# Kernel optimization log

Measured on AMD Instinct MI355X. Metric: run time of the kernel, lower is better.

The kernel has to match this reference:

```python
import jax, jax.numpy as jnp
import numpy as np

NUM_BINS = 10
BIN_DISP = 0.5
MIN_REG = 1e-5
H = 22
W = 22
S = 16
C = 256
F_ = H * W


def _distance_map(center, sz):
    # DiMP DistanceMap: soft-binned radial distance from center. [bins, sz0, sz1]
    bins = jnp.arange(NUM_BINS, dtype=jnp.float32)[:, None, None]
    k0 = jnp.arange(sz[0], dtype=jnp.float32)[:, None]
    k1 = jnp.arange(sz[1], dtype=jnp.float32)[None, :]
    dist = jnp.sqrt((k0 - center[0]) ** 2 + (k1 - center[1]) ** 2)
    bd = dist[None] / BIN_DISP - bins
    lower = jax.nn.relu(1.0 - jnp.abs(bd[:-1]))
    last = jnp.clip(1.0 + bd[-1:], 0.0, 1.0)
    return jnp.concatenate([lower, last], axis=0)


def _unfold_map(fm, h, w):
    # Equivalent of F.unfold(full_map,(h,w)).view(h,w,h,w).flip((2,3)).permute(2,3,0,1):
    # out[f=(li,lj), ki, kj] = fm[h-1-li+ki, w-1-lj+kj]
    r = (h - 1 - jnp.arange(h))[:, None] + jnp.arange(h)[None, :]  # [li, ki]
    c = (w - 1 - jnp.arange(w))[:, None] + jnp.arange(w)[None, :]  # [lj, kj]
    m = fm[r[:, None, :, None], c[None, :, None, :]]  # [li, lj, ki, kj]
    return m.reshape(h * w, h, w)


def setup_inputs() -> dict:
    key = jax.random.key(0)
    k1, k2 = jax.random.split(key)
    filt = jax.random.normal(k1, (S, F_, C, 1, 1), jnp.float32) * 0.1
    feat = jax.random.normal(k2, (1, S, C, H, W), jnp.float32)
    d = jnp.arange(NUM_BINS, dtype=jnp.float32) * BIN_DISP
    init_gauss = jnp.exp(-0.5 * d ** 2)  # init_gauss_sigma = 1.0
    return {
        "filt": filt,
        "feat": feat,
        "log_step_length": jnp.zeros((1,), jnp.float32),          # log(1.0)
        "filter_reg": 0.01 * jnp.ones((1,), jnp.float32),
        "label_w": init_gauss - init_gauss.min(),                  # label_map_predictor weights
        "mask_w": 4.0 * jnp.tanh(2.0 - d),                         # target_mask_predictor weights
        "spatial_w": jnp.ones((NUM_BINS,), jnp.float32),           # spatial_weight_predictor weights
        "num_iter": 3,
    }


def _forward(filt, feat, log_step_length, filter_reg, label_w, mask_w, spatial_w, num_iter):
    f2 = feat[0]            # [S, C, H, W]
    w = filt[..., 0, 0]     # [S, F, C]   (1x1 DiCor filters)
    h, wd = feat.shape[-2], feat.shape[-1]
    s, fnum = w.shape[0], w.shape[1]
    sz = (2 * h - 1, 2 * wd - 1)
    center = jnp.array([sz[0] // 2, sz[1] // 2], dtype=jnp.float32)
    dmap = _distance_map(center, sz)  # [bins, 2H-1, 2W-1]
    # 1x1 convs over the bin dimension, then unfold into per-filter maps [F, H, W]
    label_map = _unfold_map(jnp.einsum('bhw,b->hw', dmap, label_w), h, wd)
    target_mask = _unfold_map(jax.nn.sigmoid(jnp.einsum('bhw,b->hw', dmap, mask_w)), h, wd)
    spatial_weight = _unfold_map(jnp.einsum('bhw,b->hw', dmap, spatial_w), h, wd)
    step_length = jnp.exp(log_step_length[0])
    reg_weight = jnp.maximum(filter_reg[0] * filter_reg[0], MIN_REG ** 2)
    a = target_mask
    sw2 = spatial_weight * spatial_weight
    for _ in range(num_iter):
        # apply_filter with 1x1 filters: scores[s,f,h,w] = sum_c feat[s,c,h,w] * w[s,f,c]
        scores = jnp.einsum('schw,sfc->sfhw', f2, w)
        # LeakyReluPar / LeakyReluParDeriv with per-location slope a
        scores_act = 0.5 * (1.0 - a) * jnp.abs(scores) + 0.5 * (1.0 + a) * scores
        score_mask = 0.5 * (1.0 - a) * jnp.sign(scores) + 0.5 * (1.0 + a)
        residuals = score_mask * (sw2 * (scores_act - label_map))
        # apply_feat_transpose with 1x1 filters
        w_grad = jnp.einsum('sfhw,schw->sfc', residuals, f2) + reg_weight * w
        scores_grad = jnp.einsum('schw,sfc->sfhw', f2, w_grad)
        scores_grad = spatial_weight * (score_mask * scores_grad)
        alpha_num = jnp.sum(w_grad * w_grad, axis=2)  # [S, F]
        alpha_den = jnp.maximum(
            jnp.sum((scores_grad * scores_grad).reshape(s, fnum, -1), axis=2)
            + reg_weight * alpha_num, 1e-8)
        alpha = alpha_num / alpha_den
        w = w - step_length * alpha[..., None] * w_grad
    return w[..., None, None]  # [S, F, C, 1, 1]


def reference(filt, feat, log_step_length, filter_reg, label_w, mask_w, spatial_w, num_iter):
    return _forward(filt, feat, log_step_length, filter_reg, label_w, mask_w, spatial_w, num_iter)
```

## Files before the change

kernel.cpp:

```cpp
#include <hip/hip_runtime.h>
#include <math.h>
#include <stdint.h>

#define Ww 22
#define P_ 484
#define S_ 16
#define C_ 256
#define MP2 234256
#define TSZ 1849

typedef _Float16 f16x8 __attribute__((ext_vector_type(8)));
typedef _Float16 f16x4 __attribute__((ext_vector_type(4)));
typedef float f32x4 __attribute__((ext_vector_type(4)));

__device__ __forceinline__ int xcd_chunk(int bid, int chunk) {
    return (bid & 7) * chunk + (bid >> 3);
}

__device__ __forceinline__ void gld16(const _Float16* g, _Float16* lds) {
    auto* lp = (__attribute__((address_space(3))) uint32_t*)(uintptr_t)(lds);
    auto* gp = (const __attribute__((address_space(1))) uint32_t*)(uintptr_t)(g);
    __builtin_amdgcn_global_load_lds(gp, lp, 16, 0, 0);
}

__global__ void k_maps(const float* __restrict__ label_w, const float* __restrict__ mask_w,
                       const float* __restrict__ spatial_w, f32x4* __restrict__ map4t) {
    int idx = blockIdx.x * blockDim.x + threadIdx.x;
    if (idx >= TSZ) return;
    int dx = idx / 43 - 21, dy = idx % 43 - 21;
    float d = sqrtf((float)(dx * dx + dy * dy)) * 2.0f;
    float lab = 0.f, msk = 0.f, spw = 0.f;
#pragma unroll
    for (int b = 0; b < 9; ++b) {
        float wb = fmaxf(0.f, 1.f - fabsf(d - (float)b));
        lab += wb * label_w[b];
        msk += wb * mask_w[b];
        spw += wb * spatial_w[b];
    }
    float w9 = fminf(fmaxf(1.f + (d - 9.f), 0.f), 1.f);
    lab += w9 * label_w[9];
    msk += w9 * mask_w[9];
    spw += w9 * spatial_w[9];
    f32x4 o;
    o[0] = lab;
    o[1] = 1.f / (1.f + expf(-msk));
    o[2] = spw * spw;
    o[3] = spw;
    map4t[idx] = o;
}

__global__ __launch_bounds__(256) void k_winit(const float* __restrict__ filt,
                                               float* __restrict__ Wf, _Float16* __restrict__ Wh,
                                               float* __restrict__ num, float* __restrict__ den) {
    int wgid = xcd_chunk(blockIdx.x, 256);
    int s = wgid >> 7;
    int t = threadIdx.x;
    int f = (wgid & 127) * 4 + (t >> 6);
    int c = (t & 63) * 4;
    size_t oh = ((size_t)(s * 512 + f)) * C_ + c;
    if (f < P_) {
        size_t o = ((size_t)(s * P_ + f)) * C_ + c;
        f32x4 v = *(const f32x4*)(filt + o);
        *(f32x4*)(Wf + o) = v;
        f16x4 h;
#pragma unroll
        for (int q = 0; q < 4; ++q) h[q] = (_Float16)v[q];
        *(f16x4*)(Wh + oh) = h;
        if ((t & 63) == 0) { num[s * P_ + f] = 0.f; den[s * P_ + f] = 0.f; }
    } else {
        f16x4 h = {};
        *(f16x4*)(Wh + oh) = h;
    }
}

__global__ __launch_bounds__(256) void k_trans(const float* __restrict__ feat,
                                               _Float16* __restrict__ f2h,
                                               _Float16* __restrict__ f2th) {
    int wgid = xcd_chunk(blockIdx.x, 256);
    int s = wgid >> 7;
    int rem = wgid & 127;
    int p0 = (rem & 15) * 32, c0 = (rem >> 4) * 32;
    int cc = threadIdx.x & 31, rr = threadIdx.x >> 5;
    __shared__ float tb[32][33];
#pragma unroll
    for (int q = 0; q < 4; ++q) {
        int c = c0 + rr + q * 8;
        int p = p0 + cc;
        float v = (p < P_) ? feat[((size_t)s * C_ + c) * P_ + p] : 0.f;
        f2h[((size_t)s * C_ + c) * 512 + p] = (_Float16)v;
        tb[rr + q * 8][cc] = v;
    }
    __syncthreads();
#pragma unroll
    for (int q = 0; q < 4; ++q) {
        int p = p0 + rr + q * 8;
        f2th[((size_t)s * 512 + p) * C_ + c0 + cc] = (_Float16)tb[cc][rr + q * 8];
    }
}

template <int EPI, int KK, int LDA, int LDB, int TPS, int NBN>
__global__ __launch_bounds__(256, 4) void k_gemm(
    const _Float16* __restrict__ Ah, const _Float16* __restrict__ Bh,
    const f32x4* __restrict__ map4t, const _Float16* __restrict__ maskh_i,
    const _Float16* __restrict__ Wh_i, const float* __restrict__ freg,
    _Float16* __restrict__ out_h, _Float16* __restrict__ out_h2,
    float* __restrict__ red) {
    constexpr int TI = 2, TJ = 2, NT = KK / 128;
    int tid = threadIdx.x;
    int w = tid >> 6, l = tid & 63;
    int wgid = xcd_chunk(blockIdx.x, S_ * TPS / 8);
    int s = wgid / TPS;
    int rem = wgid % TPS;
    int m0 = (rem / NBN) * 64, n0 = (rem % NBN) * 64;
    int wm = w >> 1, wn = w & 1;
    int r16 = l & 15;

    __shared__ _Float16 As[64 * 128];
    __shared__ _Float16 Bs[64 * 128];

    int lrow = w * 4 + (l >> 4);
    int gsrc = ((l & 15) ^ lrow) << 3;
    const _Float16* gA = Ah + (size_t)s * (512 * LDA) + (size_t)(m0 + lrow) * LDA + gsrc;
    const _Float16* gB = Bh + (size_t)s * 131072 + (size_t)(n0 + lrow) * LDB + gsrc;

    f32x4 acc[TI][TJ] = {};

#pragma unroll
    for (int t = 0; t < NT; ++t) {
#pragma unroll
        for (int i = 0; i < 4; ++i) {
            gld16(gA + (size_t)i * 16 * LDA + t * 128, &As[(i * 16 + w * 4) * 128]);
            gld16(gB + (size_t)i * 16 * LDB + t * 128, &Bs[(i * 16 + w * 4) * 128]);
        }
        __syncthreads();
#pragma unroll
        for (int kk = 0; kk < 4; ++kk) {
            int px = ((kk * 4 + (l >> 4)) ^ r16) << 3;
            f16x8 af[TI], bf[TJ];
#pragma unroll
            for (int ti = 0; ti < TI; ++ti)
                af[ti] = *(const f16x8*)&As[(wm * 32 + ti * 16 + r16) * 128 + px];
#pragma unroll
            for (int tj = 0; tj < TJ; ++tj)
                bf[tj] = *(const f16x8*)&Bs[(wn * 32 + tj * 16 + r16) * 128 + px];
#pragma unroll
            for (int ti = 0; ti < TI; ++ti)
#pragma unroll
                for (int tj = 0; tj < TJ; ++tj)
                    acc[ti][tj] = __builtin_amdgcn_mfma_f32_16x16x32_f16(
                        af[ti], bf[tj], acc[ti][tj], 0, 0, 0);
        }
        if (t + 1 < NT) __syncthreads();
    }

    int q4 = (l >> 4) * 4;

    if constexpr (EPI == 1) {
#pragma unroll
        for (int ti = 0; ti < TI; ++ti)
#pragma unroll
            for (int r = 0; r < 4; ++r) {
                int m = m0 + wm * 32 + ti * 16 + q4 + r;
                int im = m / 22, jm = m - im * 22;
#pragma unroll
                for (int tj = 0; tj < TJ; ++tj) {
                    int n = n0 + wn * 32 + tj * 16 + r16;
                    float res = 0.f;
                    if (m < P_ && n < P_) {
                        int kn = n / 22, ln = n - kn * 22;
                        f32x4 m4 = map4t[(kn - im + 21) * 43 + (ln - jm + 21)];
                        float sc = acc[ti][tj][r];
                        float sgn = (sc > 0.f) ? 1.f : ((sc < 0.f) ? -1.f : 0.f);
                        float msk = 0.5f * (1.f - m4[1]) * sgn + 0.5f * (1.f + m4[1]);
                        res = msk * (m4[2] * (msk * sc - m4[0]));
                        out_h2[(size_t)s * MP2 + (size_t)m * P_ + n] = (_Float16)msk;
                    }
                    out_h[((size_t)(s * 512 + m)) * 512 + n] = (_Float16)res;
                }
            }
    } else if constexpr (EPI == 2) {
        float fr = freg[0];
        float regw = fmaxf(fr * fr, 1e-10f);
#pragma unroll
        for (int ti = 0; ti < TI; ++ti)
#pragma unroll
            for (int r = 0; r < 4; ++r) {
                int m = m0 + wm * 32 + ti * 16 + q4 + r;
                float v = 0.f;
#pragma unroll
                for (int tj = 0; tj < TJ; ++tj) {
                    int n = n0 + wn * 32 + tj * 16 + r16;
                    size_t o = ((size_t)(s * 512 + m)) * C_ + n;
                    float wg = acc[ti][tj][r] + regw * (float)Wh_i[o];
                    out_h[o] = (_Float16)wg;
                    v += wg * wg;
                }
                v += __shfl_xor(v, 1);
                v += __shfl_xor(v, 2);
                v += __shfl_xor(v, 4);
                v += __shfl_xor(v, 8);
                if (r16 == 0 && m < P_) atomicAdd(&red[s * P_ + m], v);
            }
    } else {
#pragma unroll
        for (int ti = 0; ti < TI; ++ti)
#pragma unroll
            for (int r = 0; r < 4; ++r) {
                int m = m0 + wm * 32 + ti * 16 + q4 + r;
                int im = m / 22, jm = m - im * 22;
                float v = 0.f;
#pragma unroll
                for (int tj = 0; tj < TJ; ++tj) {
                    int n = n0 + wn * 32 + tj * 16 + r16;
                    if (m < P_ && n < P_) {
                        int kn = n / 22, ln = n - kn * 22;
                        float spw = map4t[(kn - im + 21) * 43 + (ln - jm + 21)][3];
                        float msk = (float)maskh_i[(size_t)s * MP2 + (size_t)m * P_ + n];
                        float sg = spw * msk * acc[ti][tj][r];
                        v += sg * sg;
                    }
                }
                v += __shfl_xor(v, 1);
                v += __shfl_xor(v, 2);
                v += __shfl_xor(v, 4);
                v += __shfl_xor(v, 8);
                if (r16 == 0 && m < P_) atomicAdd(&red[s * P_ + m], v);
            }
    }
}

__global__ __launch_bounds__(256) void k_update(float* __restrict__ Wf,
                                                const _Float16* __restrict__ wgradh,
                                                float* __restrict__ num, float* __restrict__ den,
                                                const float* __restrict__ freg,
                                                const float* __restrict__ lsl,
                                                _Float16* __restrict__ Wh) {
    int wgid = xcd_chunk(blockIdx.x, 242);
    int s = wgid / 121;
    int t = threadIdx.x;
    int f = (wgid % 121) * 4 + (t >> 6);
    int row = s * P_ + f;
    float nu = num[row], de = den[row];
    float fr = freg[0];
    float regw = fmaxf(fr * fr, 1e-10f);
    float alpha = nu / fmaxf(de + regw * nu, 1e-8f);
    float sa = expf(lsl[0]) * alpha;
    int c = (t & 63) * 4;
    size_t o = (size_t)row * C_ + c;
    size_t oh = ((size_t)(s * 512 + f)) * C_ + c;
    f32x4 wv = *(const f32x4*)(Wf + o);
    f16x4 g = *(const f16x4*)(wgradh + oh);
    f16x4 h;
#pragma unroll
    for (int q = 0; q < 4; ++q) {
        wv[q] -= sa * (float)g[q];
        h[q] = (_Float16)wv[q];
    }
    *(f32x4*)(Wf + o) = wv;
    *(f16x4*)(Wh + oh) = h;
    if ((t & 63) == 0) { num[row] = 0.f; den[row] = 0.f; }
}

extern "C" void kernel_launch(void* const* d_in, const int* in_sizes, int n_in,
                              void* d_out, int out_size, void* d_ws, size_t ws_size,
                              hipStream_t stream) {
    const float* filt = (const float*)d_in[0];
    const float* feat = (const float*)d_in[1];
    const float* lsl  = (const float*)d_in[2];
    const float* freg = (const float*)d_in[3];
    const float* lw   = (const float*)d_in[4];
    const float* mw   = (const float*)d_in[5];
    const float* sw   = (const float*)d_in[6];
    float* Wf = (float*)d_out;

    char* ws = (char*)d_ws;
    f32x4* map4t     = (f32x4*)ws;      ws += (size_t)TSZ * 16;
    _Float16* residh = (_Float16*)ws;   ws += (size_t)S_ * 512 * 512 * 2;
    _Float16* wgradh = (_Float16*)ws;   ws += (size_t)S_ * 512 * C_ * 2;
    _Float16* Wh     = (_Float16*)ws;   ws += (size_t)S_ * 512 * C_ * 2;
    _Float16* f2h    = (_Float16*)ws;   ws += (size_t)S_ * C_ * 512 * 2;
    _Float16* f2th   = (_Float16*)ws;   ws += (size_t)S_ * 512 * C_ * 2;
    _Float16* maskh  = (_Float16*)ws;   ws += (size_t)S_ * MP2 * 2;
    float* num       = (float*)ws;      ws += (size_t)S_ * P_ * 4;
    float* den       = (float*)ws;      ws += (size_t)S_ * P_ * 4;

    k_maps<<<8, 256, 0, stream>>>(lw, mw, sw, map4t);
    k_winit<<<2048, 256, 0, stream>>>(filt, Wf, Wh, num, den);
    k_trans<<<2048, 256, 0, stream>>>(feat, f2h, f2th);

    for (int it = 0; it < 3; ++it) {
        k_gemm<1, 256, 256, 256, 64, 8><<<1024, 256, 0, stream>>>(
            Wh, f2th, map4t, nullptr, nullptr, nullptr, residh, maskh, nullptr);
        k_gemm<2, 512, 512, 512, 32, 4><<<512, 256, 0, stream>>>(
            residh, f2h, map4t, nullptr, Wh, freg, wgradh, nullptr, num);
        k_gemm<3, 256, 256, 256, 64, 8><<<1024, 256, 0, stream>>>(
            wgradh, f2th, map4t, maskh, nullptr, nullptr, nullptr, nullptr, den);
        k_update<<<1936, 256, 0, stream>>>(Wf, wgradh, num, den, freg, lsl, Wh);
    }
}
```

Measured before the change: 140.1 us.

## Update scores linearly from raw score gradient instead of recomputing score GEMM

Because scores are linear in the filter, the new scores after a step equal the old scores minus step*alpha times the raw scores_grad GEMM output, which is already computed. The code stores raw scores and raw score gradients in fp16 and updates scores elementwise in a fused update kernel, which also recomputes the mask and residual. This removes two of the three score GEMMs. The three prologue kernels are merged into one launch, and num/den use ping-pong buffers. In exchange it writes and reads several extra 512x512 fp16 planes per sequence, and fp16 rounding error can accumulate in the score updates.

```diff
diff --git a/kernel.cpp b/kernel.cpp
--- a/kernel.cpp
+++ b/kernel.cpp
@@ -6,7 +6,6 @@
 #define P_ 484
 #define S_ 16
 #define C_ 256
-#define MP2 234256
 #define TSZ 1849
 
 typedef _Float16 f16x8 __attribute__((ext_vector_type(8)));
@@ -23,12 +22,8 @@
     __builtin_amdgcn_global_load_lds(gp, lp, 16, 0, 0);
 }
 
-__global__ void k_maps(const float* __restrict__ label_w, const float* __restrict__ mask_w,
-                       const float* __restrict__ spatial_w, f32x4* __restrict__ map4t) {
-    int idx = blockIdx.x * blockDim.x + threadIdx.x;
-    if (idx >= TSZ) return;
-    int dx = idx / 43 - 21, dy = idx % 43 - 21;
-    float d = sqrtf((float)(dx * dx + dy * dy)) * 2.0f;
+__device__ __forceinline__ f32x4 map_entry(const float* label_w, const float* mask_w,
+                                           const float* spatial_w, float d) {
     float lab = 0.f, msk = 0.f, spw = 0.f;
 #pragma unroll
     for (int b = 0; b < 9; ++b) {
@@ -46,65 +41,78 @@
     o[1] = 1.f / (1.f + expf(-msk));
     o[2] = spw * spw;
     o[3] = spw;
-    map4t[idx] = o;
-}
-
-__global__ __launch_bounds__(256) void k_winit(const float* __restrict__ filt,
-                                               float* __restrict__ Wf, _Float16* __restrict__ Wh,
-                                               float* __restrict__ num, float* __restrict__ den) {
-    int wgid = xcd_chunk(blockIdx.x, 256);
-    int s = wgid >> 7;
+    return o;
+}
+
+__global__ __launch_bounds__(256) void k_pro(
+    const float* __restrict__ filt, const float* __restrict__ feat,
+    const float* __restrict__ lw, const float* __restrict__ mw,
+    const float* __restrict__ sw,
+    float* __restrict__ Wf, _Float16* __restrict__ Wh,
+    float* __restrict__ num0, float* __restrict__ den0,
+    _Float16* __restrict__ f2h, _Float16* __restrict__ f2th,
+    f32x4* __restrict__ map4t) {
+    int wgid = xcd_chunk(blockIdx.x, 514);
+    int x = wgid / 514;
+    int local = wgid % 514;
     int t = threadIdx.x;
-    int f = (wgid & 127) * 4 + (t >> 6);
-    int c = (t & 63) * 4;
-    size_t oh = ((size_t)(s * 512 + f)) * C_ + c;
-    if (f < P_) {
-        size_t o = ((size_t)(s * P_ + f)) * C_ + c;
-        f32x4 v = *(const f32x4*)(filt + o);
-        *(f32x4*)(Wf + o) = v;
-        f16x4 h;
-#pragma unroll
-        for (int q = 0; q < 4; ++q) h[q] = (_Float16)v[q];
-        *(f16x4*)(Wh + oh) = h;
-        if ((t & 63) == 0) { num[s * P_ + f] = 0.f; den[s * P_ + f] = 0.f; }
-    } else {
-        f16x4 h = {};
-        *(f16x4*)(Wh + oh) = h;
-    }
-}
-
-__global__ __launch_bounds__(256) void k_trans(const float* __restrict__ feat,
-                                               _Float16* __restrict__ f2h,
-                                               _Float16* __restrict__ f2th) {
-    int wgid = xcd_chunk(blockIdx.x, 256);
-    int s = wgid >> 7;
-    int rem = wgid & 127;
-    int p0 = (rem & 15) * 32, c0 = (rem >> 4) * 32;
-    int cc = threadIdx.x & 31, rr = threadIdx.x >> 5;
-    __shared__ float tb[32][33];
-#pragma unroll
-    for (int q = 0; q < 4; ++q) {
-        int c = c0 + rr + q * 8;
-        int p = p0 + cc;
-        float v = (p < P_) ? feat[((size_t)s * C_ + c) * P_ + p] : 0.f;
-        f2h[((size_t)s * C_ + c) * 512 + p] = (_Float16)v;
-        tb[rr + q * 8][cc] = v;
-    }
-    __syncthreads();
-#pragma unroll
-    for (int q = 0; q < 4; ++q) {
-        int p = p0 + rr + q * 8;
-        f2th[((size_t)s * 512 + p) * C_ + c0 + cc] = (_Float16)tb[cc][rr + q * 8];
-    }
-}
-
-template <int EPI, int KK, int LDA, int LDB, int TPS, int NBN>
+    if (local == 0) {
+        int idx = x + 8 * t;
+        if (idx < TSZ) {
+            int dx = idx / 43 - 21, dy = idx % 43 - 21;
+            float d = sqrtf((float)(dx * dx + dy * dy)) * 2.0f;
+            map4t[idx] = map_entry(lw, mw, sw, d);
+        }
+    } else if (local < 257) {
+        int u = local - 1;
+        int s = x * 2 + (u >> 7);
+        int f = (u & 127) * 4 + (t >> 6);
+        int c = (t & 63) * 4;
+        size_t oh = ((size_t)(s * 512 + f)) * C_ + c;
+        if (f < P_) {
+            size_t o = ((size_t)(s * P_ + f)) * C_ + c;
+            f32x4 v = *(const f32x4*)(filt + o);
+            *(f32x4*)(Wf + o) = v;
+            f16x4 h;
+#pragma unroll
+            for (int q = 0; q < 4; ++q) h[q] = (_Float16)v[q];
+            *(f16x4*)(Wh + oh) = h;
+            if ((t & 63) == 0) { num0[s * P_ + f] = 0.f; den0[s * P_ + f] = 0.f; }
+        } else {
+            f16x4 h = {};
+            *(f16x4*)(Wh + oh) = h;
+        }
+    } else if (local < 513) {
+        int u = local - 257;
+        int s = x * 2 + (u >> 7);
+        int rem = u & 127;
+        int p0 = (rem & 15) * 32, c0 = (rem >> 4) * 32;
+        int cc = t & 31, rr = t >> 5;
+        __shared__ float tb[32][33];
+#pragma unroll
+        for (int q = 0; q < 4; ++q) {
+            int c = c0 + rr + q * 8;
+            int p = p0 + cc;
+            float v = (p < P_) ? feat[((size_t)s * C_ + c) * P_ + p] : 0.f;
+            f2h[((size_t)s * C_ + c) * 512 + p] = (_Float16)v;
+            tb[rr + q * 8][cc] = v;
+        }
+        __syncthreads();
+#pragma unroll
+        for (int q = 0; q < 4; ++q) {
+            int p = p0 + rr + q * 8;
+            f2th[((size_t)s * 512 + p) * C_ + c0 + cc] = (_Float16)tb[cc][rr + q * 8];
+        }
+    }
+}
+
+template <int EPI, int KK, int LDA, int LDB, int TPS, int NBN, bool WSG = false>
 __global__ __launch_bounds__(256, 4) void k_gemm(
     const _Float16* __restrict__ Ah, const _Float16* __restrict__ Bh,
     const f32x4* __restrict__ map4t, const _Float16* __restrict__ maskh_i,
     const _Float16* __restrict__ Wh_i, const float* __restrict__ freg,
     _Float16* __restrict__ out_h, _Float16* __restrict__ out_h2,
-    float* __restrict__ red) {
+    _Float16* __restrict__ out_h3, float* __restrict__ red) {
     constexpr int TI = 2, TJ = 2, NT = KK / 128;
     int tid = threadIdx.x;
     int w = tid >> 6, l = tid & 63;
@@ -165,17 +173,19 @@
 #pragma unroll
                 for (int tj = 0; tj < TJ; ++tj) {
                     int n = n0 + wn * 32 + tj * 16 + r16;
+                    float sc = acc[ti][tj][r];
                     float res = 0.f;
+                    size_t po = ((size_t)(s * 512 + m)) * 512 + n;
                     if (m < P_ && n < P_) {
                         int kn = n / 22, ln = n - kn * 22;
                         f32x4 m4 = map4t[(kn - im + 21) * 43 + (ln - jm + 21)];
-                        float sc = acc[ti][tj][r];
                         float sgn = (sc > 0.f) ? 1.f : ((sc < 0.f) ? -1.f : 0.f);
                         float msk = 0.5f * (1.f - m4[1]) * sgn + 0.5f * (1.f + m4[1]);
                         res = msk * (m4[2] * (msk * sc - m4[0]));
-                        out_h2[(size_t)s * MP2 + (size_t)m * P_ + n] = (_Float16)msk;
+                        out_h2[po] = (_Float16)msk;
                     }
-                    out_h[((size_t)(s * 512 + m)) * 512 + n] = (_Float16)res;
+                    out_h[po] = (_Float16)res;
+                    out_h3[po] = (_Float16)sc;
                 }
             }
     } else if constexpr (EPI == 2) {
@@ -212,11 +222,14 @@
 #pragma unroll
                 for (int tj = 0; tj < TJ; ++tj) {
                     int n = n0 + wn * 32 + tj * 16 + r16;
+                    float sc = acc[ti][tj][r];
+                    if constexpr (WSG)
+                        out_h[((size_t)(s * 512 + m)) * 512 + n] = (_Float16)sc;
                     if (m < P_ && n < P_) {
                         int kn = n / 22, ln = n - kn * 22;
                         float spw = map4t[(kn - im + 21) * 43 + (ln - jm + 21)][3];
-                        float msk = (float)maskh_i[(size_t)s * MP2 + (size_t)m * P_ + n];
-                        float sg = spw * msk * acc[ti][tj][r];
+                        float msk = (float)maskh_i[((size_t)(s * 512 + m)) * 512 + n];
+                        float sg = spw * msk * sc;
                         v += sg * sg;
                     }
                 }
@@ -229,12 +242,80 @@
     }
 }
 
+__global__ __launch_bounds__(256) void k_fu(
+    float* __restrict__ Wf, _Float16* __restrict__ Wh,
+    const _Float16* __restrict__ wgradh,
+    const float* __restrict__ num_rd, const float* __restrict__ den_rd,
+    float* __restrict__ num_zw, float* __restrict__ den_zw,
+    const _Float16* __restrict__ sgrawh, _Float16* __restrict__ scoresh,
+    _Float16* __restrict__ residh, _Float16* __restrict__ maskh,
+    const f32x4* __restrict__ map4t,
+    const float* __restrict__ freg, const float* __restrict__ lsl) {
+    int wgid = xcd_chunk(blockIdx.x, 484);
+    int s = wgid / 242;
+    int local = wgid % 242;
+    int t = threadIdx.x;
+    float fr = freg[0];
+    float regw = fmaxf(fr * fr, 1e-10f);
+    float step = expf(lsl[0]);
+    if (local < 121) {
+        int f = local * 4 + (t >> 6);
+        int row = s * P_ + f;
+        float nu = num_rd[row], de = den_rd[row];
+        float sa = step * (nu / fmaxf(de + regw * nu, 1e-8f));
+        int c = (t & 63) * 4;
+        size_t o = (size_t)row * C_ + c;
+        size_t oh = ((size_t)(s * 512 + f)) * C_ + c;
+        f32x4 wv = *(const f32x4*)(Wf + o);
+        f16x4 g = *(const f16x4*)(wgradh + oh);
+        f16x4 h;
+#pragma unroll
+        for (int q = 0; q < 4; ++q) {
+            wv[q] -= sa * (float)g[q];
+            h[q] = (_Float16)wv[q];
+        }
+        *(f32x4*)(Wf + o) = wv;
+        *(f16x4*)(Wh + oh) = h;
+        if ((t & 63) == 0) { num_zw[row] = 0.f; den_zw[row] = 0.f; }
+    } else {
+        int m = (local - 121) * 4 + (t >> 6);
+        int row = s * P_ + m;
+        float nu = num_rd[row], de = den_rd[row];
+        float sa = step * (nu / fmaxf(de + regw * nu, 1e-8f));
+        int im = m / 22, jm = m - im * 22;
+        int n0 = (t & 63) * 8;
+        size_t ro = ((size_t)(s * 512 + m)) * 512 + n0;
+        f16x8 so = *(const f16x8*)(scoresh + ro);
+        f16x8 gg = *(const f16x8*)(sgrawh + ro);
+        f16x8 sn, rs, mk;
+#pragma unroll
+        for (int j = 0; j < 8; ++j) {
+            float sc = (float)so[j] - sa * (float)gg[j];
+            sn[j] = (_Float16)sc;
+            int n = n0 + j;
+            float res = 0.f, msk = 0.f;
+            if (n < P_) {
+                int kn = n / 22, ln = n - kn * 22;
+                f32x4 m4 = map4t[(kn - im + 21) * 43 + (ln - jm + 21)];
+                float sgn = (sc > 0.f) ? 1.f : ((sc < 0.f) ? -1.f : 0.f);
+                msk = 0.5f * (1.f - m4[1]) * sgn + 0.5f * (1.f + m4[1]);
+                res = msk * (m4[2] * (msk * sc - m4[0]));
+            }
+            rs[j] = (_Float16)res;
+            mk[j] = (_Float16)msk;
+        }
+        *(f16x8*)(scoresh + ro) = sn;
+        *(f16x8*)(residh + ro) = rs;
+        *(f16x8*)(maskh + ro) = mk;
+    }
+}
+
 __global__ __launch_bounds__(256) void k_update(float* __restrict__ Wf,
                                                 const _Float16* __restrict__ wgradh,
-                                                float* __restrict__ num, float* __restrict__ den,
+                                                const float* __restrict__ num,
+                                                const float* __restrict__ den,
                                                 const float* __restrict__ freg,
-                                                const float* __restrict__ lsl,
-                                                _Float16* __restrict__ Wh) {
+                                                const float* __restrict__ lsl) {
     int wgid = xcd_chunk(blockIdx.x, 242);
     int s = wgid / 121;
     int t = threadIdx.x;
@@ -243,22 +324,15 @@
     float nu = num[row], de = den[row];
     float fr = freg[0];
     float regw = fmaxf(fr * fr, 1e-10f);
-    float alpha = nu / fmaxf(de + regw * nu, 1e-8f);
-    float sa = expf(lsl[0]) * alpha;
+    float sa = expf(lsl[0]) * (nu / fmaxf(de + regw * nu, 1e-8f));
     int c = (t & 63) * 4;
     size_t o = (size_t)row * C_ + c;
     size_t oh = ((size_t)(s * 512 + f)) * C_ + c;
     f32x4 wv = *(const f32x4*)(Wf + o);
     f16x4 g = *(const f16x4*)(wgradh + oh);
-    f16x4 h;
-#pragma unroll
-    for (int q = 0; q < 4; ++q) {
-        wv[q] -= sa * (float)g[q];
-        h[q] = (_Float16)wv[q];
-    }
+#pragma unroll
+    for (int q = 0; q < 4; ++q) wv[q] -= sa * (float)g[q];
     *(f32x4*)(Wf + o) = wv;
-    *(f16x4*)(Wh + oh) = h;
-    if ((t & 63) == 0) { num[row] = 0.f; den[row] = 0.f; }
 }
 
 extern "C" void kernel_launch(void* const* d_in, const int* in_sizes, int n_in,
@@ -276,25 +350,38 @@
     char* ws = (char*)d_ws;
     f32x4* map4t     = (f32x4*)ws;      ws += (size_t)TSZ * 16;
     _Float16* residh = (_Float16*)ws;   ws += (size_t)S_ * 512 * 512 * 2;
+    _Float16* scoresh= (_Float16*)ws;   ws += (size_t)S_ * 512 * 512 * 2;
+    _Float16* sgrawh = (_Float16*)ws;   ws += (size_t)S_ * 512 * 512 * 2;
+    _Float16* maskh  = (_Float16*)ws;   ws += (size_t)S_ * 512 * 512 * 2;
     _Float16* wgradh = (_Float16*)ws;   ws += (size_t)S_ * 512 * C_ * 2;
     _Float16* Wh     = (_Float16*)ws;   ws += (size_t)S_ * 512 * C_ * 2;
     _Float16* f2h    = (_Float16*)ws;   ws += (size_t)S_ * C_ * 512 * 2;
     _Float16* f2th   = (_Float16*)ws;   ws += (size_t)S_ * 512 * C_ * 2;
-    _Float16* maskh  = (_Float16*)ws;   ws += (size_t)S_ * MP2 * 2;
-    float* num       = (float*)ws;      ws += (size_t)S_ * P_ * 4;
-    float* den       = (float*)ws;      ws += (size_t)S_ * P_ * 4;
-
-    k_maps<<<8, 256, 0, stream>>>(lw, mw, sw, map4t);
-    k_winit<<<2048, 256, 0, stream>>>(filt, Wf, Wh, num, den);
-    k_trans<<<2048, 256, 0, stream>>>(feat, f2h, f2th);
-
-    for (int it = 0; it < 3; ++it) {
-        k_gemm<1, 256, 256, 256, 64, 8><<<1024, 256, 0, stream>>>(
-            Wh, f2th, map4t, nullptr, nullptr, nullptr, residh, maskh, nullptr);
-        k_gemm<2, 512, 512, 512, 32, 4><<<512, 256, 0, stream>>>(
-            residh, f2h, map4t, nullptr, Wh, freg, wgradh, nullptr, num);
-        k_gemm<3, 256, 256, 256, 64, 8><<<1024, 256, 0, stream>>>(
-            wgradh, f2th, map4t, maskh, nullptr, nullptr, nullptr, nullptr, den);
-        k_update<<<1936, 256, 0, stream>>>(Wf, wgradh, num, den, freg, lsl, Wh);
-    }
-}
+    float* num0      = (float*)ws;      ws += (size_t)S_ * P_ * 4;
+    float* den0      = (float*)ws;      ws += (size_t)S_ * P_ * 4;
+    float* num1      = (float*)ws;      ws += (size_t)S_ * P_ * 4;
+    float* den1      = (float*)ws;      ws += (size_t)S_ * P_ * 4;
+
+    k_pro<<<4112, 256, 0, stream>>>(filt, feat, lw, mw, sw, Wf, Wh, num0, den0,
+                                    f2h, f2th, map4t);
+
+    k_gemm<1, 256, 256, 256, 64, 8><<<1024, 256, 0, stream>>>(
+        Wh, f2th, map4t, nullptr, nullptr, nullptr, residh, maskh, scoresh, nullptr);
+    k_gemm<2, 512, 512, 512, 32, 4><<<512, 256, 0, stream>>>(
+        residh, f2h, map4t, nullptr, Wh, freg, wgradh, nullptr, nullptr, num0);
+    k_gemm<3, 256, 256, 256, 64, 8, true><<<1024, 256, 0, stream>>>(
+        wgradh, f2th, map4t, maskh, nullptr, nullptr, sgrawh, nullptr, nullptr, den0);
+    k_fu<<<3872, 256, 0, stream>>>(Wf, Wh, wgradh, num0, den0, num1, den1,
+                                   sgrawh, scoresh, residh, maskh, map4t, freg, lsl);
+    k_gemm<2, 512, 512, 512, 32, 4><<<512, 256, 0, stream>>>(
+        residh, f2h, map4t, nullptr, Wh, freg, wgradh, nullptr, nullptr, num1);
+    k_gemm<3, 256, 256, 256, 64, 8, true><<<1024, 256, 0, stream>>>(
+        wgradh, f2th, map4t, maskh, nullptr, nullptr, sgrawh, nullptr, nullptr, den1);
+    k_fu<<<3872, 256, 0, stream>>>(Wf, Wh, wgradh, num1, den1, num0, den0,
+                                   sgrawh, scoresh, residh, maskh, map4t, freg, lsl);
+    k_gemm<2, 512, 512, 512, 32, 4><<<512, 256, 0, stream>>>(
+        residh, f2h, map4t, nullptr, Wh, freg, wgradh, nullptr, nullptr, num0);
+    k_gemm<3, 256, 256, 256, 64, 8, false><<<1024, 256, 0, stream>>>(
+        wgradh, f2th, map4t, maskh, nullptr, nullptr, nullptr, nullptr, nullptr, den0);
+    k_update<<<1936, 256, 0, stream>>>(Wf, wgradh, num0, den0, freg, lsl);
+}
```

New measurement: 129.1 us. -7.9%, faster.
